# Kernel optimization log

Hardware: AMD Instinct MI355X
Metric: run time of the kernel (lower is better)

The kernel has to match this reference:

```python
import jax, jax.numpy as jnp
import numpy as np

B, T, D, H, TW = 4, 2048, 2048, 8, 4
DH = D // H


def setup_inputs() -> dict:
    key = jax.random.key(0)
    ks = jax.random.split(key, 16)
    s = lambda k, shape, std: jax.random.normal(k, shape, dtype=jnp.float32) * std
    inp = {
        "x": jax.random.normal(ks[0], (B, T, D), dtype=jnp.float32),
        "segment_pos": jnp.tile(jnp.arange(T, dtype=jnp.int32), (B, 1)),
        # linear_y / linear_x: width -> lru_width, std = 1/sqrt(width)
        "Wy": s(ks[1], (D, D), (1.0 / D) ** 0.5),
        "by": jnp.zeros((D,), jnp.float32),
        "Wx": s(ks[2], (D, D), (1.0 / D) ** 0.5),
        "bx": jnp.zeros((D,), jnp.float32),
        # depthwise causal conv: [temporal_width, lru_width]
        "conv_w": s(ks[3], (TW, D), (1.0 / TW) ** 0.5),
        "conv_b": jnp.zeros((D,), jnp.float32),
        # RG-LRU block-diagonal gates: [H, D/H, D/H]
        "gx_w": s(ks[4], (H, DH, DH), (1.0 / DH) ** 0.5),
        "gx_b": jnp.zeros((H, DH), jnp.float32),
        "ga_w": s(ks[5], (H, DH, DH), (1.0 / DH) ** 0.5),
        "ga_b": jnp.zeros((H, DH), jnp.float32),
        # a_param: softplus(a_param) > 0 controls decay rate
        "a_param": jnp.log(jnp.exp(jax.random.uniform(ks[6], (D,), minval=0.3, maxval=0.9)) - 1.0 + 1e-6),
        # linear_out: lru_width -> width, std = 1/sqrt(lru_width)
        "Wout": s(ks[7], (D, D), (1.0 / D) ** 0.5),
        "bout": jnp.zeros((D,), jnp.float32),
    }
    return inp


def _causal_conv1d(x, w, b, segment_pos):
    # depthwise causal conv over time; contributions from other segments masked
    t = x.shape[1]
    acc = jnp.zeros_like(x)
    for i in range(TW):
        shift = TW - 1 - i  # input at t - shift, weighted by w[i]
        xs = x if shift == 0 else jnp.pad(x, ((0, 0), (shift, 0), (0, 0)))[:, :t]
        mask = (segment_pos >= shift)[..., None].astype(x.dtype)
        acc = acc + xs * mask * w[i]
    return acc + b


def _rg_lru(x, segment_pos, gx_w, gx_b, ga_w, ga_b, a_param):
    b, t, d = x.shape
    xr = x.reshape(b, t, H, DH)
    gate_x = jax.nn.sigmoid(jnp.einsum("bthi,hij->bthj", xr, gx_w) + gx_b).reshape(b, t, d)
    gate_a = jax.nn.sigmoid(jnp.einsum("bthi,hij->bthj", xr, ga_w) + ga_b).reshape(b, t, d)
    log_a = -8.0 * gate_a * jax.nn.softplus(a_param)  # [B,T,D]
    a = jnp.exp(log_a)
    reset = (segment_pos == 0)[..., None]  # [B,T,1]
    multiplier = jnp.sqrt(jnp.maximum(1.0 - jnp.exp(2.0 * log_a), 0.0))
    multiplier = jnp.where(reset, 1.0, multiplier)
    normed = x * gate_x * multiplier
    a_scan = jnp.where(reset, 0.0, a)

    def step(h, inputs):
        a_t, x_t = inputs
        h = a_t * h + x_t
        return h, h

    h0 = jnp.zeros((b, d), x.dtype)
    _, ys = jax.lax.scan(step, h0, (a_scan.transpose(1, 0, 2), normed.transpose(1, 0, 2)))
    return ys.transpose(1, 0, 2)


def reference(x, segment_pos, Wy, by, Wx, bx, conv_w, conv_b, gx_w, gx_b, ga_w, ga_b, a_param, Wout, bout):
    y = jax.nn.gelu(x @ Wy.T + by, approximate=True)
    x_proj = x @ Wx.T + bx
    x_conv = _causal_conv1d(x_proj, conv_w, conv_b, segment_pos)
    x_lru = _rg_lru(x_conv, segment_pos, gx_w, gx_b, ga_w, ga_b, a_param)
    out = (x_lru * y) @ Wout.T + bout
    return out
```

## Files before the change

kernel.cpp:

```cpp
#include <hip/hip_runtime.h>
#include <cstdint>
#include <cstddef>

typedef __bf16 bf16;
typedef __bf16 bf16x8 __attribute__((ext_vector_type(8)));
typedef float f32x4 __attribute__((ext_vector_type(4)));

#define BDIM 4
#define TDIM 2048
#define DDIM 2048
#define HDIM 8
#define DHD 256
#define MTOT 8192
#define NCHUNK 64
#define LCHUNK 32

__device__ __forceinline__ void stage16(const bf16* g, bf16* l) {
  __builtin_amdgcn_global_load_lds(
      (const __attribute__((address_space(1))) void*)g,
      (__attribute__((address_space(3))) void*)l, 16, 0, 0);
}

#define SBAR() asm volatile("s_barrier" ::: "memory")
#define WAITVM(N) asm volatile("s_waitcnt vmcnt(" #N ")" ::: "memory")
#define LGKM0() asm volatile("s_waitcnt lgkmcnt(0)" ::: "memory")

__device__ __forceinline__ float sigmoid_f(float x) {
  return __fdividef(1.f, 1.f + __expf(-x));
}
__device__ __forceinline__ float gelu_tanh(float v) {
  float u = 0.7978845608028654f * (v + 0.044715f * v * v * v);
  u = fminf(fmaxf(u, -15.f), 15.f);
  float t = __expf(2.f * u);
  return 0.5f * v * (1.f + __fdividef(t - 1.f, t + 1.f));
}
__device__ __forceinline__ float softplus_f(float x) {
  return __logf(1.f + __expf(x));
}

__global__ __launch_bounds__(256) void f2b(const float* __restrict__ src,
                                           bf16* __restrict__ dst) {
  size_t i = ((size_t)blockIdx.x * 256 + threadIdx.x) * 8;
  const float4 a = *(const float4*)(src + i);
  const float4 b = *(const float4*)(src + i + 4);
  bf16x8 r;
  r[0] = (bf16)a.x; r[1] = (bf16)a.y; r[2] = (bf16)a.z; r[3] = (bf16)a.w;
  r[4] = (bf16)b.x; r[5] = (bf16)b.y; r[6] = (bf16)b.z; r[7] = (bf16)b.w;
  *(bf16x8*)(dst + i) = r;
}

template <typename TO, int EPI>
__global__ __launch_bounds__(512, 2) void gemm256(
    const bf16* __restrict__ A, const bf16* __restrict__ Bm,
    const float* __restrict__ bias, TO* __restrict__ C,
    int K, int lda, int ldb, int ldc) {
  const int gx = gridDim.x, gy = gridDim.y;
  const int nwg = gx * gy;
  const int did = blockIdx.x + gx * blockIdx.y;
  const int cpx = nwg >> 3;
  const int lid = (did & 7) * cpx + (did >> 3);
  const int n0 = (lid % gx) * 256;
  const int m0 = (lid / gx) * 256;

  __shared__ bf16 sA[2][256][64];
  __shared__ bf16 sB[2][256][64];
  const int tid = threadIdx.x;
  const int lane = tid & 63;
  const int wid = tid >> 6;
  const int wr = wid >> 2;
  const int wc = wid & 3;
  const int quad = lane >> 4;
  const int l15 = lane & 15;

  const int sr = tid >> 3;
  const int ks8 = ((tid & 7) ^ (sr & 7)) << 3;
  const bf16* Ag = A + (size_t)(m0 + sr) * lda + ks8;
  const bf16* Bg = Bm + (size_t)(n0 + sr) * ldb + ks8;

  const int swz0 = ((quad) ^ (l15 & 7)) << 3;
  const int swz1 = ((4 + quad) ^ (l15 & 7)) << 3;

  f32x4 acc[8][4];
#pragma unroll
  for (int i = 0; i < 8; ++i)
#pragma unroll
    for (int j = 0; j < 4; ++j)
#pragma unroll
      for (int r = 0; r < 4; ++r) acc[i][j][r] = 0.f;

  const int NT = K >> 6;

#define STAGE_A(P, TK)                                                        \
  do {                                                                        \
    const size_t ko_ = (size_t)(TK) << 6;                                     \
    _Pragma("unroll") for (int c_ = 0; c_ < 4; ++c_)                          \
        stage16(Ag + (size_t)(c_ * 64) * lda + ko_,                           \
                &sA[P][c_ * 64 + wid * 8][0]);                                \
  } while (0)
#define STAGE_B(P, TK)                                                        \
  do {                                                                        \
    const size_t ko_ = (size_t)(TK) << 6;                                     \
    _Pragma("unroll") for (int c_ = 0; c_ < 4; ++c_)                          \
        stage16(Bg + (size_t)(c_ * 64) * ldb + ko_,                           \
                &sB[P][c_ * 64 + wid * 8][0]);                                \
  } while (0)

  bf16x8 afr[2][4][2], bfr[2][2][2];

#define READ_A(MH)                                                            \
  do {                                                                        \
    _Pragma("unroll") for (int mi_ = 0; mi_ < 4; ++mi_) {                     \
      const int arow_ = wr * 128 + (MH) * 64 + mi_ * 16 + l15;                \
      afr[MH][mi_][0] = *(const bf16x8*)(As0 + arow_ * 64 + swz0);            \
      afr[MH][mi_][1] = *(const bf16x8*)(As0 + arow_ * 64 + swz1);            \
    }                                                                         \
  } while (0)
#define READ_B(NH)                                                            \
  do {                                                                        \
    _Pragma("unroll") for (int ni_ = 0; ni_ < 2; ++ni_) {                     \
      const int brow_ = wc * 64 + (NH) * 32 + ni_ * 16 + l15;                 \
      bfr[NH][ni_][0] = *(const bf16x8*)(Bs0 + brow_ * 64 + swz0);            \
      bfr[NH][ni_][1] = *(const bf16x8*)(Bs0 + brow_ * 64 + swz1);            \
    }                                                                         \
  } while (0)
#define MFMA_QUAD(MH, NH)                                                     \
  do {                                                                        \
    __builtin_amdgcn_s_setprio(1);                                            \
    _Pragma("unroll") for (int mi_ = 0; mi_ < 4; ++mi_)                       \
        _Pragma("unroll") for (int ni_ = 0; ni_ < 2; ++ni_) {                 \
      acc[(MH)*4 + mi_][(NH)*2 + ni_] = __builtin_amdgcn_mfma_f32_16x16x32_bf16( \
          afr[MH][mi_][0], bfr[NH][ni_][0], acc[(MH)*4 + mi_][(NH)*2 + ni_], 0, 0, 0); \
      acc[(MH)*4 + mi_][(NH)*2 + ni_] = __builtin_amdgcn_mfma_f32_16x16x32_bf16( \
          afr[MH][mi_][1], bfr[NH][ni_][1], acc[(MH)*4 + mi_][(NH)*2 + ni_], 0, 0, 0); \
    }                                                                         \
    __builtin_amdgcn_s_setprio(0);                                            \
  } while (0)

  STAGE_A(0, 0);
  STAGE_B(0, 0);
  STAGE_A(1, 1);
  STAGE_B(1, 1);

  int p = 0;
  for (int t = 0; t < NT; ++t) {
    if (t == NT - 1) { WAITVM(0); } else { WAITVM(8); }
    SBAR();
    const bf16* As0 = &sA[p][0][0];
    const bf16* Bs0 = &sB[p][0][0];
    READ_A(0);
    READ_B(0);
    SBAR();
    MFMA_QUAD(0, 0);
    SBAR();
    READ_A(1);
    READ_B(1);
    LGKM0();
    __builtin_amdgcn_sched_barrier(0);
    SBAR();
    MFMA_QUAD(0, 1);
    SBAR();
    if (t + 2 < NT) STAGE_A(p, t + 2);
    MFMA_QUAD(1, 0);
    SBAR();
    if (t + 2 < NT) STAGE_B(p, t + 2);
    MFMA_QUAD(1, 1);
    p ^= 1;
  }

#undef STAGE_A
#undef STAGE_B
#undef READ_A
#undef READ_B
#undef MFMA_QUAD

#pragma unroll
  for (int nn = 0; nn < 4; ++nn) {
    const int n = n0 + wc * 64 + nn * 16 + l15;
    const float bv = bias[n];
#pragma unroll
    for (int mm = 0; mm < 8; ++mm) {
#pragma unroll
      for (int r = 0; r < 4; ++r) {
        const int m = m0 + wr * 128 + mm * 16 + quad * 4 + r;
        float v = acc[mm][nn][r] + bv;
        if (EPI == 1) v = gelu_tanh(v);
        C[(size_t)m * ldc + n] = (TO)v;
      }
    }
  }
}

__global__ __launch_bounds__(256) void gate_gemm(
    const bf16* __restrict__ xconv,
    const bf16* __restrict__ gxT, const bf16* __restrict__ gaT,
    bf16* __restrict__ gxr, bf16* __restrict__ gar) {
  const int h = blockIdx.z >> 1;
  const int g = blockIdx.z & 1;
  const bf16* A = xconv + h * DHD;
  const bf16* Bm = (g ? gaT : gxT) + (size_t)h * DHD * DHD;
  bf16* C = (g ? gar : gxr) + h * DHD;
  const int n0 = blockIdx.x * 128;
  const int m0 = blockIdx.y * 128;
  __shared__ bf16 As[128 * 32];
  __shared__ bf16 Bs[128 * 32];
  const int tid = threadIdx.x;
  const int lane = tid & 63;
  const int wid = tid >> 6;
  const int waveM = wid >> 1, waveN = wid & 1;
  const int quad = lane >> 4;
  const int l15 = lane & 15;
  const int srow = lane >> 2;
  const int scol = (lane & 3) * 8;

  f32x4 acc[4][4];
#pragma unroll
  for (int i = 0; i < 4; ++i)
#pragma unroll
    for (int j = 0; j < 4; ++j)
#pragma unroll
      for (int r = 0; r < 4; ++r) acc[i][j][r] = 0.f;

  for (int k0 = 0; k0 < DHD; k0 += 32) {
    if (k0) __syncthreads();
#pragma unroll
    for (int cc = 0; cc < 2; ++cc) {
      const int q = wid * 2 + cc;
      const int row = q * 16 + srow;
      stage16(A + (size_t)(m0 + row) * DDIM + k0 + scol, As + q * 512);
      stage16(Bm + (size_t)(n0 + row) * DHD + k0 + scol, Bs + q * 512);
    }
    __syncthreads();
    bf16x8 af[4], bfr[4];
#pragma unroll
    for (int i = 0; i < 4; ++i) {
      af[i]  = *(const bf16x8*)&As[(waveM * 64 + i * 16 + l15) * 32 + quad * 8];
      bfr[i] = *(const bf16x8*)&Bs[(waveN * 64 + i * 16 + l15) * 32 + quad * 8];
    }
#pragma unroll
    for (int i = 0; i < 4; ++i)
#pragma unroll
      for (int j = 0; j < 4; ++j)
        acc[i][j] = __builtin_amdgcn_mfma_f32_16x16x32_bf16(af[i], bfr[j], acc[i][j], 0, 0, 0);
  }

#pragma unroll
  for (int j = 0; j < 4; ++j) {
    const int n = n0 + waveN * 64 + j * 16 + l15;
#pragma unroll
    for (int i = 0; i < 4; ++i) {
#pragma unroll
      for (int r = 0; r < 4; ++r) {
        const int m = m0 + waveM * 64 + i * 16 + quad * 4 + r;
        C[(size_t)m * DDIM + n] = (bf16)acc[i][j][r];
      }
    }
  }
}

__global__ __launch_bounds__(256) void conv_kernel(
    const bf16* __restrict__ xp, const float* __restrict__ cw,
    const float* __restrict__ cb, const int* __restrict__ segp,
    bf16* __restrict__ xc) {
  int v = blockIdx.x * 256 + threadIdx.x;
  int dv = v & (DDIM / 8 - 1);
  int m = v >> 8;
  int d0 = dv * 8;
  int t = m & (TDIM - 1);
  int sp = segp[m];
  float acc[8];
#pragma unroll
  for (int j = 0; j < 8; ++j) acc[j] = cb[d0 + j];
#pragma unroll
  for (int i = 0; i < 4; ++i) {
    int shift = 3 - i;
    if (t >= shift && sp >= shift) {
      bf16x8 xv = *(const bf16x8*)&xp[(size_t)(m - shift) * DDIM + d0];
#pragma unroll
      for (int j = 0; j < 8; ++j) acc[j] = fmaf((float)xv[j], cw[i * DDIM + d0 + j], acc[j]);
    }
  }
  bf16x8 o;
#pragma unroll
  for (int j = 0; j < 8; ++j) o[j] = (bf16)acc[j];
  *(bf16x8*)&xc[(size_t)m * DDIM + d0] = o;
}

__global__ __launch_bounds__(256) void transpose_gates(
    const float* __restrict__ gxw, const float* __restrict__ gaw,
    bf16* __restrict__ gxT, bf16* __restrict__ gaT) {
  __shared__ bf16 tile[32][33];
  int zz = blockIdx.z;
  int h = zz >> 1;
  const float* src = (zz & 1) ? gaw : gxw;
  bf16* dst = (zz & 1) ? gaT : gxT;
  int j0 = blockIdx.x * 32;
  int i0 = blockIdx.y * 32;
  int r = threadIdx.x >> 5;
  int c = threadIdx.x & 31;
  for (int rr = r; rr < 32; rr += 8)
    tile[rr][c] = (bf16)src[(size_t)(h * DHD + i0 + rr) * DHD + j0 + c];
  __syncthreads();
  for (int rr = r; rr < 32; rr += 8)
    dst[(size_t)(h * DHD + j0 + rr) * DHD + i0 + c] = tile[c][rr];
}

__device__ __forceinline__ void lru_elem(float pgx, float pga, float xc,
                                         float spv, bool reset,
                                         float& a, float& nr) {
  const float gx = sigmoid_f(pgx);
  const float ga = sigmoid_f(pga);
  const float la = -8.f * ga * spv;
  a = reset ? 0.f : __expf(la);
  const float mult = reset ? 1.f : sqrtf(fmaxf(1.f - __expf(2.f * la), 0.f));
  nr = xc * gx * mult;
}

__global__ __launch_bounds__(256) void scan_phase1(
    const bf16* __restrict__ gxr, const bf16* __restrict__ gar,
    const bf16* __restrict__ xconv,
    const float* __restrict__ gxb, const float* __restrict__ gab,
    const float* __restrict__ apar, const int* __restrict__ segp,
    float* __restrict__ chA, float* __restrict__ chH) {
  int idx = blockIdx.x * 256 + threadIdx.x;
  int d = idx & (DDIM - 1);
  int c = (idx >> 11) & (NCHUNK - 1);
  int b = idx >> 17;
  const float gxbv = gxb[d], gabv = gab[d];
  const float spv = softplus_f(apar[d]);
  const int mrow = b * TDIM + c * LCHUNK;
  size_t base = (size_t)mrow * DDIM + d;
  float A = 1.f, hh = 0.f;
  for (int i = 0; i < LCHUNK; ++i) {
    size_t o = base + (size_t)i * DDIM;
    float a, nr;
    lru_elem((float)gxr[o] + gxbv, (float)gar[o] + gabv, (float)xconv[o],
             spv, segp[mrow + i] == 0, a, nr);
    hh = fmaf(a, hh, nr);
    A *= a;
  }
  int ci = (b * NCHUNK + c) * DDIM + d;
  chA[ci] = A;
  chH[ci] = hh;
}

__global__ __launch_bounds__(256) void scan_phase2(
    const float* __restrict__ chA, const float* __restrict__ chH,
    float* __restrict__ hst) {
  int idx = blockIdx.x * 256 + threadIdx.x;
  int d = idx & (DDIM - 1);
  int b = idx >> 11;
  float s = 0.f;
  for (int c = 0; c < NCHUNK; ++c) {
    int ci = (b * NCHUNK + c) * DDIM + d;
    hst[ci] = s;
    s = fmaf(chA[ci], s, chH[ci]);
  }
}

__global__ __launch_bounds__(256) void scan_phase3(
    const bf16* __restrict__ gxr, const bf16* __restrict__ gar,
    const bf16* __restrict__ xconv,
    const float* __restrict__ gxb, const float* __restrict__ gab,
    const float* __restrict__ apar, const int* __restrict__ segp,
    const float* __restrict__ hst, bf16* __restrict__ yz) {
  int idx = blockIdx.x * 256 + threadIdx.x;
  int d = idx & (DDIM - 1);
  int c = (idx >> 11) & (NCHUNK - 1);
  int b = idx >> 17;
  const float gxbv = gxb[d], gabv = gab[d];
  const float spv = softplus_f(apar[d]);
  const int mrow = b * TDIM + c * LCHUNK;
  size_t base = (size_t)mrow * DDIM + d;
  float hh = hst[(b * NCHUNK + c) * DDIM + d];
  for (int i = 0; i < LCHUNK; ++i) {
    size_t o = base + (size_t)i * DDIM;
    float a, nr;
    lru_elem((float)gxr[o] + gxbv, (float)gar[o] + gabv, (float)xconv[o],
             spv, segp[mrow + i] == 0, a, nr);
    hh = fmaf(a, hh, nr);
    yz[o] = (bf16)(hh * (float)yz[o]);
  }
}

extern "C" void kernel_launch(void* const* d_in, const int* in_sizes, int n_in,
                              void* d_out, int out_size, void* d_ws, size_t ws_size,
                              hipStream_t stream) {
  const float* x    = (const float*)d_in[0];
  const int*   segp = (const int*)d_in[1];
  const float* Wy   = (const float*)d_in[2];
  const float* by   = (const float*)d_in[3];
  const float* Wx   = (const float*)d_in[4];
  const float* bx   = (const float*)d_in[5];
  const float* cw   = (const float*)d_in[6];
  const float* cb   = (const float*)d_in[7];
  const float* gxw  = (const float*)d_in[8];
  const float* gxb  = (const float*)d_in[9];
  const float* gaw  = (const float*)d_in[10];
  const float* gab  = (const float*)d_in[11];
  const float* apar = (const float*)d_in[12];
  const float* Wout = (const float*)d_in[13];
  const float* bout = (const float*)d_in[14];

  const size_t MD = (size_t)MTOT * DDIM;
  const size_t WD = (size_t)DDIM * DDIM;
  bf16* xb    = (bf16*)d_out;
  bf16* xproj = (bf16*)((char*)d_out + MD * 2);
  bf16* xconv = xb;
  bf16* gxr   = xproj;

  char* ws = (char*)d_ws;
  bf16*  gar = (bf16*)ws;
  bf16*  W1  = (bf16*)(ws + MD * 2);
  bf16*  WB1 = (bf16*)(ws + 2 * MD * 2);
  bf16*  WB2 = (bf16*)(ws + 2 * MD * 2 + WD * 2);
  char*  tail = ws + 2 * MD * 2 + 2 * WD * 2;
  const size_t GW = (size_t)HDIM * DHD * DHD * 2;
  const size_t CH = (size_t)BDIM * NCHUNK * DDIM * 4;
  bf16*  gxT = (bf16*)tail;
  bf16*  gaT = (bf16*)(tail + GW);
  float* chA = (float*)(tail + 2 * GW);
  float* chH = (float*)(tail + 2 * GW + CH);
  float* hst = (float*)(tail + 2 * GW + 2 * CH);

  dim3 blk(256);
  f2b<<<dim3(MD / 2048), blk, 0, stream>>>(x, xb);
  f2b<<<dim3(WD / 2048), blk, 0, stream>>>(Wx, WB1);
  f2b<<<dim3(WD / 2048), blk, 0, stream>>>(Wy, WB2);
  transpose_gates<<<dim3(8, 8, 16), blk, 0, stream>>>(gxw, gaw, gxT, gaT);

  gemm256<bf16, 0><<<dim3(8, 32), dim3(512), 0, stream>>>(xb, WB1, bx, xproj, DDIM, DDIM, DDIM, DDIM);
  gemm256<bf16, 1><<<dim3(8, 32), dim3(512), 0, stream>>>(xb, WB2, by, W1, DDIM, DDIM, DDIM, DDIM);

  conv_kernel<<<dim3(MTOT * (DDIM / 8) / 256), blk, 0, stream>>>(xproj, cw, cb, segp, xconv);

  gate_gemm<<<dim3(2, 64, 16), blk, 0, stream>>>(xconv, gxT, gaT, gxr, gar);

  scan_phase1<<<dim3(BDIM * NCHUNK * DDIM / 256), blk, 0, stream>>>(
      gxr, gar, xconv, gxb, gab, apar, segp, chA, chH);
  scan_phase2<<<dim3(BDIM * DDIM / 256), blk, 0, stream>>>(chA, chH, hst);
  scan_phase3<<<dim3(BDIM * NCHUNK * DDIM / 256), blk, 0, stream>>>(
      gxr, gar, xconv, gxb, gab, apar, segp, hst, W1);

  f2b<<<dim3(WD / 2048), blk, 0, stream>>>(Wout, WB1);
  gemm256<float, 0><<<dim3(8, 32), dim3(512), 0, stream>>>(W1, WB1, bout, (float*)d_out, DDIM, DDIM, DDIM, DDIM);
}
```

Baseline: 420.5 us.

## Reschedule GEMM main loop to hold half the A fragments and batch staging

The GEMM main loop now keeps only one half of the A fragments in registers and reuses the two B fragment sets across both A halves. MFMAs are reordered as (0,0), (0,1), (1,0), (1,1), with the second A half read between them. Both global-to-LDS stages for tile t+2 are issued together, and the vmcnt wait plus barrier move to the end of each iteration. The aim is lower VGPR pressure, which may help occupancy or reduce spills, and better overlap of LDS reads with MFMAs. The cost is extra barriers per iteration and a different load/compute overlap pattern.

```diff
diff --git a/kernel.cpp b/kernel.cpp
--- a/kernel.cpp
+++ b/kernel.cpp
@@ -105,33 +105,33 @@
                 &sB[P][c_ * 64 + wid * 8][0]);                                \
   } while (0)
 
-  bf16x8 afr[2][4][2], bfr[2][2][2];
+  bf16x8 afr[4][2], b0r[2][2], b1r[2][2];
 
 #define READ_A(MH)                                                            \
   do {                                                                        \
     _Pragma("unroll") for (int mi_ = 0; mi_ < 4; ++mi_) {                     \
       const int arow_ = wr * 128 + (MH) * 64 + mi_ * 16 + l15;                \
-      afr[MH][mi_][0] = *(const bf16x8*)(As0 + arow_ * 64 + swz0);            \
-      afr[MH][mi_][1] = *(const bf16x8*)(As0 + arow_ * 64 + swz1);            \
+      afr[mi_][0] = *(const bf16x8*)(As0 + arow_ * 64 + swz0);                \
+      afr[mi_][1] = *(const bf16x8*)(As0 + arow_ * 64 + swz1);                \
     }                                                                         \
   } while (0)
-#define READ_B(NH)                                                            \
+#define READ_B(NH, DST)                                                       \
   do {                                                                        \
     _Pragma("unroll") for (int ni_ = 0; ni_ < 2; ++ni_) {                     \
       const int brow_ = wc * 64 + (NH) * 32 + ni_ * 16 + l15;                 \
-      bfr[NH][ni_][0] = *(const bf16x8*)(Bs0 + brow_ * 64 + swz0);            \
-      bfr[NH][ni_][1] = *(const bf16x8*)(Bs0 + brow_ * 64 + swz1);            \
+      DST[ni_][0] = *(const bf16x8*)(Bs0 + brow_ * 64 + swz0);                \
+      DST[ni_][1] = *(const bf16x8*)(Bs0 + brow_ * 64 + swz1);                \
     }                                                                         \
   } while (0)
-#define MFMA_QUAD(MH, NH)                                                     \
+#define MFMA_Q(MH, NH, BR)                                                    \
   do {                                                                        \
     __builtin_amdgcn_s_setprio(1);                                            \
     _Pragma("unroll") for (int mi_ = 0; mi_ < 4; ++mi_)                       \
         _Pragma("unroll") for (int ni_ = 0; ni_ < 2; ++ni_) {                 \
       acc[(MH)*4 + mi_][(NH)*2 + ni_] = __builtin_amdgcn_mfma_f32_16x16x32_bf16( \
-          afr[MH][mi_][0], bfr[NH][ni_][0], acc[(MH)*4 + mi_][(NH)*2 + ni_], 0, 0, 0); \
+          afr[mi_][0], BR[ni_][0], acc[(MH)*4 + mi_][(NH)*2 + ni_], 0, 0, 0); \
       acc[(MH)*4 + mi_][(NH)*2 + ni_] = __builtin_amdgcn_mfma_f32_16x16x32_bf16( \
-          afr[MH][mi_][1], bfr[NH][ni_][1], acc[(MH)*4 + mi_][(NH)*2 + ni_], 0, 0, 0); \
+          afr[mi_][1], BR[ni_][1], acc[(MH)*4 + mi_][(NH)*2 + ni_], 0, 0, 0); \
     }                                                                         \
     __builtin_amdgcn_s_setprio(0);                                            \
   } while (0)
@@ -140,30 +140,35 @@
   STAGE_B(0, 0);
   STAGE_A(1, 1);
   STAGE_B(1, 1);
+  WAITVM(8);
+  SBAR();
 
   int p = 0;
   for (int t = 0; t < NT; ++t) {
-    if (t == NT - 1) { WAITVM(0); } else { WAITVM(8); }
-    SBAR();
     const bf16* As0 = &sA[p][0][0];
     const bf16* Bs0 = &sB[p][0][0];
     READ_A(0);
-    READ_B(0);
-    SBAR();
-    MFMA_QUAD(0, 0);
+    READ_B(0, b0r);
+    SBAR();
+    MFMA_Q(0, 0, b0r);
+    SBAR();
+    READ_B(1, b1r);
+    SBAR();
+    MFMA_Q(0, 1, b1r);
     SBAR();
     READ_A(1);
-    READ_B(1);
+    SBAR();
+    MFMA_Q(1, 0, b0r);
     LGKM0();
     __builtin_amdgcn_sched_barrier(0);
     SBAR();
-    MFMA_QUAD(0, 1);
-    SBAR();
-    if (t + 2 < NT) STAGE_A(p, t + 2);
-    MFMA_QUAD(1, 0);
-    SBAR();
-    if (t + 2 < NT) STAGE_B(p, t + 2);
-    MFMA_QUAD(1, 1);
+    if (t + 2 < NT) {
+      STAGE_A(p, t + 2);
+      STAGE_B(p, t + 2);
+    }
+    MFMA_Q(1, 1, b1r);
+    if (t + 2 < NT) { WAITVM(8); } else { WAITVM(0); }
+    SBAR();
     p ^= 1;
   }
 
@@ -171,7 +176,7 @@
 #undef STAGE_B
 #undef READ_A
 #undef READ_B
-#undef MFMA_QUAD
+#undef MFMA_Q
 
 #pragma unroll
   for (int nn = 0; nn < 4; ++nn) {
```

Result: no change. 428.1 us (+1.8%).

## Split GEMM LDS tiles into K-halves and interleave finer-grained staging with MFMAs

Applied to the files above, without the earlier changes.

Each 64-wide K tile in the bf16 GEMM is now split into two 32-wide LDS sub-buffers, with a new XOR swizzle for the global-to-LDS copies and the fragment reads. The main loop is rescheduled so that async global_load_lds copies of sub-tiles are issued between MFMA groups, with vmcnt waits and barriers at quarter-tile granularity. A-fragments are loaded once per K-half and reused across both N-halves, which cuts register use. The aim is better overlap of memory traffic with matrix math and fewer LDS bank conflicts. In exchange, the async LDS writes and the reads depend on tight wait counts, and the final iterations redundantly reload the last tile.

```diff
diff --git a/kernel.cpp b/kernel.cpp
--- a/kernel.cpp
+++ b/kernel.cpp
@@ -23,7 +23,6 @@
 
 #define SBAR() asm volatile("s_barrier" ::: "memory")
 #define WAITVM(N) asm volatile("s_waitcnt vmcnt(" #N ")" ::: "memory")
-#define LGKM0() asm volatile("s_waitcnt lgkmcnt(0)" ::: "memory")
 
 __device__ __forceinline__ float sigmoid_f(float x) {
   return __fdividef(1.f, 1.f + __expf(-x));
@@ -62,8 +61,8 @@
   const int n0 = (lid % gx) * 256;
   const int m0 = (lid / gx) * 256;
 
-  __shared__ bf16 sA[2][256][64];
-  __shared__ bf16 sB[2][256][64];
+  __shared__ bf16 sA[2][2][256][32];
+  __shared__ bf16 sB[2][2][256][32];
   const int tid = threadIdx.x;
   const int lane = tid & 63;
   const int wid = tid >> 6;
@@ -72,13 +71,14 @@
   const int quad = lane >> 4;
   const int l15 = lane & 15;
 
-  const int sr = tid >> 3;
-  const int ks8 = ((tid & 7) ^ (sr & 7)) << 3;
-  const bf16* Ag = A + (size_t)(m0 + sr) * lda + ks8;
-  const bf16* Bg = Bm + (size_t)(n0 + sr) * ldb + ks8;
-
-  const int swz0 = ((quad) ^ (l15 & 7)) << 3;
-  const int swz1 = ((4 + quad) ^ (l15 & 7)) << 3;
+  const int slot = (quad ^ (l15 & 3) ^ ((l15 >> 2) & 3)) * 8;
+  const int aoff = (wr * 128 + l15) * 32 + slot;
+  const int boff = (wc * 64 + l15) * 32 + slot;
+
+  const int rg = wid * 32 + (lane >> 2);
+  const int kx = ((lane & 3) ^ (rg & 3) ^ ((rg >> 2) & 3)) * 8;
+  const bf16* AgS = A + (size_t)(m0 + rg) * lda + kx;
+  const bf16* BgS = Bm + (size_t)(n0 + rg) * ldb + kx;
 
   f32x4 acc[8][4];
 #pragma unroll
@@ -90,88 +90,78 @@
 
   const int NT = K >> 6;
 
-#define STAGE_A(P, TK)                                                        \
+#define STA(P, KS, TK)                                                        \
   do {                                                                        \
-    const size_t ko_ = (size_t)(TK) << 6;                                     \
-    _Pragma("unroll") for (int c_ = 0; c_ < 4; ++c_)                          \
-        stage16(Ag + (size_t)(c_ * 64) * lda + ko_,                           \
-                &sA[P][c_ * 64 + wid * 8][0]);                                \
+    _Pragma("unroll") for (int j_ = 0; j_ < 2; ++j_)                          \
+        stage16(AgS + (size_t)j_ * 16 * lda + (TK) * 64 + (KS) * 32,          \
+                &sA[P][KS][wid * 32 + j_ * 16][0]);                           \
   } while (0)
-#define STAGE_B(P, TK)                                                        \
+#define STB(P, KS, TK)                                                        \
   do {                                                                        \
-    const size_t ko_ = (size_t)(TK) << 6;                                     \
-    _Pragma("unroll") for (int c_ = 0; c_ < 4; ++c_)                          \
-        stage16(Bg + (size_t)(c_ * 64) * ldb + ko_,                           \
-                &sB[P][c_ * 64 + wid * 8][0]);                                \
+    _Pragma("unroll") for (int j_ = 0; j_ < 2; ++j_)                          \
+        stage16(BgS + (size_t)j_ * 16 * ldb + (TK) * 64 + (KS) * 32,          \
+                &sB[P][KS][wid * 32 + j_ * 16][0]);                           \
   } while (0)
 
-  bf16x8 afr[2][4][2], bfr[2][2][2];
-
-#define READ_A(MH)                                                            \
+  bf16x8 af[8], bfr[2];
+
+#define RD_A(KS)                                                              \
   do {                                                                        \
-    _Pragma("unroll") for (int mi_ = 0; mi_ < 4; ++mi_) {                     \
-      const int arow_ = wr * 128 + (MH) * 64 + mi_ * 16 + l15;                \
-      afr[MH][mi_][0] = *(const bf16x8*)(As0 + arow_ * 64 + swz0);            \
-      afr[MH][mi_][1] = *(const bf16x8*)(As0 + arow_ * 64 + swz1);            \
-    }                                                                         \
+    _Pragma("unroll") for (int mi_ = 0; mi_ < 8; ++mi_)                       \
+        af[mi_] = *(const bf16x8*)(Ab + (KS) * 8192 + mi_ * 512);             \
   } while (0)
-#define READ_B(NH)                                                            \
+#define RD_B(KS, NH)                                                          \
   do {                                                                        \
-    _Pragma("unroll") for (int ni_ = 0; ni_ < 2; ++ni_) {                     \
-      const int brow_ = wc * 64 + (NH) * 32 + ni_ * 16 + l15;                 \
-      bfr[NH][ni_][0] = *(const bf16x8*)(Bs0 + brow_ * 64 + swz0);            \
-      bfr[NH][ni_][1] = *(const bf16x8*)(Bs0 + brow_ * 64 + swz1);            \
-    }                                                                         \
+    _Pragma("unroll") for (int ni_ = 0; ni_ < 2; ++ni_)                       \
+        bfr[ni_] = *(const bf16x8*)(Bb + (KS) * 8192 + (NH) * 1024 + ni_ * 512); \
   } while (0)
-#define MFMA_QUAD(MH, NH)                                                     \
+#define MFMA16(NH)                                                            \
   do {                                                                        \
     __builtin_amdgcn_s_setprio(1);                                            \
-    _Pragma("unroll") for (int mi_ = 0; mi_ < 4; ++mi_)                       \
-        _Pragma("unroll") for (int ni_ = 0; ni_ < 2; ++ni_) {                 \
-      acc[(MH)*4 + mi_][(NH)*2 + ni_] = __builtin_amdgcn_mfma_f32_16x16x32_bf16( \
-          afr[MH][mi_][0], bfr[NH][ni_][0], acc[(MH)*4 + mi_][(NH)*2 + ni_], 0, 0, 0); \
-      acc[(MH)*4 + mi_][(NH)*2 + ni_] = __builtin_amdgcn_mfma_f32_16x16x32_bf16( \
-          afr[MH][mi_][1], bfr[NH][ni_][1], acc[(MH)*4 + mi_][(NH)*2 + ni_], 0, 0, 0); \
-    }                                                                         \
+    _Pragma("unroll") for (int mi_ = 0; mi_ < 8; ++mi_)                       \
+        _Pragma("unroll") for (int ni_ = 0; ni_ < 2; ++ni_)                   \
+            acc[mi_][(NH)*2 + ni_] = __builtin_amdgcn_mfma_f32_16x16x32_bf16( \
+                af[mi_], bfr[ni_], acc[mi_][(NH)*2 + ni_], 0, 0, 0);          \
     __builtin_amdgcn_s_setprio(0);                                            \
   } while (0)
 
-  STAGE_A(0, 0);
-  STAGE_B(0, 0);
-  STAGE_A(1, 1);
-  STAGE_B(1, 1);
-
-  int p = 0;
+  STA(0, 0, 0); STB(0, 0, 0); STA(0, 1, 0); STB(0, 1, 0);
+  STA(1, 0, 1); STB(1, 0, 1); STA(1, 1, 1);
+  WAITVM(10);
+  SBAR();
+
   for (int t = 0; t < NT; ++t) {
-    if (t == NT - 1) { WAITVM(0); } else { WAITVM(8); }
+    const int p = t & 1;
+    const bf16* Ab = &sA[p][0][0][0] + aoff;
+    const bf16* Bb = &sB[p][0][0][0] + boff;
+    const int tk1 = (t + 1 < NT) ? t + 1 : NT - 1;
+    const int tk2 = (t + 2 < NT) ? t + 2 : NT - 1;
+    RD_A(0); RD_B(0, 0);
+    STB(p ^ 1, 1, tk1);
+    MFMA16(0);
     SBAR();
-    const bf16* As0 = &sA[p][0][0];
-    const bf16* Bs0 = &sB[p][0][0];
-    READ_A(0);
-    READ_B(0);
+    RD_B(0, 1);
+    STA(p, 0, tk2);
+    MFMA16(1);
+    WAITVM(10);
     SBAR();
-    MFMA_QUAD(0, 0);
+    RD_A(1); RD_B(1, 0);
+    STB(p, 0, tk2);
+    MFMA16(0);
     SBAR();
-    READ_A(1);
-    READ_B(1);
-    LGKM0();
-    __builtin_amdgcn_sched_barrier(0);
+    RD_B(1, 1);
+    STA(p, 1, tk2);
+    MFMA16(1);
+    WAITVM(10);
     SBAR();
-    MFMA_QUAD(0, 1);
-    SBAR();
-    if (t + 2 < NT) STAGE_A(p, t + 2);
-    MFMA_QUAD(1, 0);
-    SBAR();
-    if (t + 2 < NT) STAGE_B(p, t + 2);
-    MFMA_QUAD(1, 1);
-    p ^= 1;
-  }
-
-#undef STAGE_A
-#undef STAGE_B
-#undef READ_A
-#undef READ_B
-#undef MFMA_QUAD
+  }
+  WAITVM(0);
+
+#undef STA
+#undef STB
+#undef RD_A
+#undef RD_B
+#undef MFMA16
 
 #pragma unroll
   for (int nn = 0; nn < 4; ++nn) {
```

Measured after the change: 448.3 us. 6.6% more time.

## Restructure GEMM main loop into half-tile staged software pipeline

Applied to the files above, without the earlier changes.

Splits global-to-LDS staging of A and B tiles into halves that are issued between MFMA quadrants. The loop now prefetches register fragments for the next iteration across the loop boundary and uses compiler barrier builtins instead of inline asm barriers. The aim is to overlap LDS reads, global loads and MFMA work more finely and to cut stalls at barriers. In exchange, the vmcnt accounting is more intricate, and clamped redundant loads on the last iterations add a small amount of extra traffic.

```diff
diff --git a/kernel.cpp b/kernel.cpp
--- a/kernel.cpp
+++ b/kernel.cpp
@@ -21,9 +21,9 @@
       (__attribute__((address_space(3))) void*)l, 16, 0, 0);
 }
 
-#define SBAR() asm volatile("s_barrier" ::: "memory")
-#define WAITVM(N) asm volatile("s_waitcnt vmcnt(" #N ")" ::: "memory")
-#define LGKM0() asm volatile("s_waitcnt lgkmcnt(0)" ::: "memory")
+#define BARX() __builtin_amdgcn_s_barrier()
+#define SCHB() __builtin_amdgcn_sched_barrier(0)
+#define WAITVM(N) asm volatile("s_waitcnt vmcnt(" #N ")")
 
 __device__ __forceinline__ float sigmoid_f(float x) {
   return __fdividef(1.f, 1.f + __expf(-x));
@@ -90,88 +90,100 @@
 
   const int NT = K >> 6;
 
-#define STAGE_A(P, TK)                                                        \
+#define STA_H(P, H, TK)                                                       \
   do {                                                                        \
-    const size_t ko_ = (size_t)(TK) << 6;                                     \
-    _Pragma("unroll") for (int c_ = 0; c_ < 4; ++c_)                          \
-        stage16(Ag + (size_t)(c_ * 64) * lda + ko_,                           \
-                &sA[P][c_ * 64 + wid * 8][0]);                                \
+    _Pragma("unroll") for (int j_ = 0; j_ < 2; ++j_) {                        \
+      const int c_ = (H) * 2 + j_;                                            \
+      stage16(Ag + (size_t)(c_ * 64) * lda + (size_t)(TK) * 64,               \
+              &sA[P][c_ * 64 + wid * 8][0]);                                  \
+    }                                                                         \
   } while (0)
-#define STAGE_B(P, TK)                                                        \
+#define STB_H(P, H, TK)                                                       \
   do {                                                                        \
-    const size_t ko_ = (size_t)(TK) << 6;                                     \
-    _Pragma("unroll") for (int c_ = 0; c_ < 4; ++c_)                          \
-        stage16(Bg + (size_t)(c_ * 64) * ldb + ko_,                           \
-                &sB[P][c_ * 64 + wid * 8][0]);                                \
+    _Pragma("unroll") for (int j_ = 0; j_ < 2; ++j_) {                        \
+      const int c_ = (H) * 2 + j_;                                            \
+      stage16(Bg + (size_t)(c_ * 64) * ldb + (size_t)(TK) * 64,               \
+              &sB[P][c_ * 64 + wid * 8][0]);                                  \
+    }                                                                         \
   } while (0)
 
-  bf16x8 afr[2][4][2], bfr[2][2][2];
-
-#define READ_A(MH)                                                            \
+  bf16x8 aq0[4][2], aq1[4][2], b0[2][2], b1[2][2];
+
+#define RDA(DST, MH, BUF)                                                     \
   do {                                                                        \
+    const bf16* As_ = &sA[BUF][0][0];                                         \
     _Pragma("unroll") for (int mi_ = 0; mi_ < 4; ++mi_) {                     \
       const int arow_ = wr * 128 + (MH) * 64 + mi_ * 16 + l15;                \
-      afr[MH][mi_][0] = *(const bf16x8*)(As0 + arow_ * 64 + swz0);            \
-      afr[MH][mi_][1] = *(const bf16x8*)(As0 + arow_ * 64 + swz1);            \
+      DST[mi_][0] = *(const bf16x8*)(As_ + arow_ * 64 + swz0);                \
+      DST[mi_][1] = *(const bf16x8*)(As_ + arow_ * 64 + swz1);                \
     }                                                                         \
   } while (0)
-#define READ_B(NH)                                                            \
+#define RDB(DST, NH, BUF)                                                     \
   do {                                                                        \
+    const bf16* Bs_ = &sB[BUF][0][0];                                         \
     _Pragma("unroll") for (int ni_ = 0; ni_ < 2; ++ni_) {                     \
       const int brow_ = wc * 64 + (NH) * 32 + ni_ * 16 + l15;                 \
-      bfr[NH][ni_][0] = *(const bf16x8*)(Bs0 + brow_ * 64 + swz0);            \
-      bfr[NH][ni_][1] = *(const bf16x8*)(Bs0 + brow_ * 64 + swz1);            \
+      DST[ni_][0] = *(const bf16x8*)(Bs_ + brow_ * 64 + swz0);                \
+      DST[ni_][1] = *(const bf16x8*)(Bs_ + brow_ * 64 + swz1);                \
     }                                                                         \
   } while (0)
-#define MFMA_QUAD(MH, NH)                                                     \
+#define MFMAQ(MH, NH, AA, BB)                                                 \
   do {                                                                        \
     __builtin_amdgcn_s_setprio(1);                                            \
     _Pragma("unroll") for (int mi_ = 0; mi_ < 4; ++mi_)                       \
         _Pragma("unroll") for (int ni_ = 0; ni_ < 2; ++ni_) {                 \
       acc[(MH)*4 + mi_][(NH)*2 + ni_] = __builtin_amdgcn_mfma_f32_16x16x32_bf16( \
-          afr[MH][mi_][0], bfr[NH][ni_][0], acc[(MH)*4 + mi_][(NH)*2 + ni_], 0, 0, 0); \
+          AA[mi_][0], BB[ni_][0], acc[(MH)*4 + mi_][(NH)*2 + ni_], 0, 0, 0);  \
       acc[(MH)*4 + mi_][(NH)*2 + ni_] = __builtin_amdgcn_mfma_f32_16x16x32_bf16( \
-          afr[MH][mi_][1], bfr[NH][ni_][1], acc[(MH)*4 + mi_][(NH)*2 + ni_], 0, 0, 0); \
+          AA[mi_][1], BB[ni_][1], acc[(MH)*4 + mi_][(NH)*2 + ni_], 0, 0, 0);  \
     }                                                                         \
     __builtin_amdgcn_s_setprio(0);                                            \
   } while (0)
 
-  STAGE_A(0, 0);
-  STAGE_B(0, 0);
-  STAGE_A(1, 1);
-  STAGE_B(1, 1);
-
-  int p = 0;
+  const int t1 = (NT > 1) ? 1 : 0;
+  STB_H(0, 0, 0); STA_H(0, 0, 0);
+  STB_H(0, 1, 0); STA_H(0, 1, 0);
+  STB_H(1, 0, t1); STA_H(1, 0, t1);
+  WAITVM(8);
+  SCHB();
+  BARX();
+  RDA(aq0, 0, 0);
+  RDB(b0, 0, 0);
+
   for (int t = 0; t < NT; ++t) {
-    if (t == NT - 1) { WAITVM(0); } else { WAITVM(8); }
-    SBAR();
-    const bf16* As0 = &sA[p][0][0];
-    const bf16* Bs0 = &sB[p][0][0];
-    READ_A(0);
-    READ_B(0);
-    SBAR();
-    MFMA_QUAD(0, 0);
-    SBAR();
-    READ_A(1);
-    READ_B(1);
-    LGKM0();
-    __builtin_amdgcn_sched_barrier(0);
-    SBAR();
-    MFMA_QUAD(0, 1);
-    SBAR();
-    if (t + 2 < NT) STAGE_A(p, t + 2);
-    MFMA_QUAD(1, 0);
-    SBAR();
-    if (t + 2 < NT) STAGE_B(p, t + 2);
-    MFMA_QUAD(1, 1);
-    p ^= 1;
-  }
-
-#undef STAGE_A
-#undef STAGE_B
-#undef READ_A
-#undef READ_B
-#undef MFMA_QUAD
+    const int p = t & 1;
+    const int tn = (t + 1 < NT) ? t + 1 : NT - 1;
+    const int tnn = (t + 2 < NT) ? t + 2 : NT - 1;
+    WAITVM(4);
+    SCHB();
+    RDB(b1, 1, p);
+    STB_H(p ^ 1, 1, tn);
+    MFMAQ(0, 0, aq0, b0);
+    BARX();
+    RDA(aq1, 1, p);
+    STA_H(p ^ 1, 1, tn);
+    MFMAQ(0, 1, aq0, b1);
+    BARX();
+    STB_H(p, 0, tnn);
+    MFMAQ(1, 0, aq1, b0);
+    BARX();
+    WAITVM(6);
+    SCHB();
+    if (t + 1 < NT) {
+      RDA(aq0, 0, p ^ 1);
+      RDB(b0, 0, p ^ 1);
+    }
+    STA_H(p, 0, tnn);
+    MFMAQ(1, 1, aq1, b1);
+    BARX();
+  }
+  WAITVM(0);
+
+#undef STA_H
+#undef STB_H
+#undef RDA
+#undef RDB
+#undef MFMAQ
 
 #pragma unroll
   for (int nn = 0; nn < 4; ++nn) {
```

After: 407.3 us. -3.1%, faster.
